# Performance work log

Hardware: AMD Instinct MI355X
Metric: run time of the kernel (lower is better)

Reference implementation:

```python
import jax, jax.numpy as jnp
import numpy as np

N, C, T, V = 32, 128, 256, 25
K = 5  # temporal kernel size; reflect-pad 2*(K-1)//2 = 4 rows on top
EPS = 1e-5


def _inorm(x):
    # InstanceNorm2d(affine=False): normalize each (n,c) plane over (T,V)
    m = jnp.mean(x, axis=(2, 3), keepdims=True)
    v = jnp.var(x, axis=(2, 3), keepdims=True)
    return (x - m) * jax.lax.rsqrt(v + EPS)


def setup_inputs() -> dict:
    key = jax.random.key(0)
    ks = jax.random.split(key, 5)
    x = jax.random.normal(ks[0], (N, C, T, V), jnp.float32)
    PA = jax.random.normal(ks[1], (V, V), jnp.float32)          # learned adjacency
    Wd = jax.random.normal(ks[2], (C, C), jnp.float32) * 0.05    # 1x1 conv weight (O,I)
    bd = jnp.zeros((C,), jnp.float32)
    Wt = jax.random.normal(ks[3], (C, C, K, 1), jnp.float32) * 0.02  # (O,I,Kt,1)
    bt = jnp.zeros((C,), jnp.float32)
    return {"x": x, "PA": PA, "Wd": Wd, "bd": bd, "Wt": Wt, "bt": bt}


def reference(x, PA, Wd, bd, Wt, bt):
    # GCN unit: x.view(N,C*T,V) @ PA == einsum over last (joint) axis
    g = jnp.einsum('nctv,vw->nctw', x, PA)
    # 1x1 conv (channel GEMM) + bias
    y = jnp.einsum('nctv,oc->notv', g, Wd) + bd[None, :, None, None]
    # instance norm + identity residual (in_c == out_c) + relu
    y = jax.nn.relu(_inorm(y) + x)
    # TCN unit: reflection-pad 4 rows on top of T, conv (5,1) stride 1, instance norm
    yp = jnp.pad(y, ((0, 0), (0, 0), (4, 0), (0, 0)), mode='reflect')
    z = jax.lax.conv_general_dilated(
        yp, Wt, window_strides=(1, 1), padding='VALID',
        dimension_numbers=('NCHW', 'OIHW', 'NCHW')) + bt[None, :, None, None]
    z = _inorm(z)
    # outer residual (identity: in_c == out_c, stride == 1) + relu
    return jax.nn.relu(z + x)
```

## Files before the change

### kernel.cpp

```cpp
#include <hip/hip_runtime.h>


typedef unsigned short u16;
typedef unsigned int   u32;

using short8  = __attribute__((ext_vector_type(8))) short;
using floatx4 = __attribute__((ext_vector_type(4))) float;

#define NBATCH 32
#define CH     128
#define TDIM   256
#define VDIM   25
#define KT     5
#define PLANE  6400
#define EPSF   1e-5f
#define INV_PLANE (1.0f/6400.0f)

__device__ __forceinline__ u16 f2bf(float f) {
    u32 u = __float_as_uint(f);
    return (u16)((u + 0x7fffu + ((u >> 16) & 1u)) >> 16);
}
__device__ __forceinline__ float bf2f(u16 h) {
    return __uint_as_float(((u32)h) << 16);
}
__device__ __forceinline__ void gload_lds16(const void* g, void* l) {
    __builtin_amdgcn_global_load_lds(
        (const __attribute__((address_space(1))) u32*)g,
        (__attribute__((address_space(3))) u32*)l, 16, 0, 0);
}

__global__ __launch_bounds__(256) void k0_init(
    const float* __restrict__ Wd, const float* __restrict__ Wt,
    float* __restrict__ statsY, float* __restrict__ statsZ,
    u16* __restrict__ WdB, u16* __restrict__ Wt_b)
{
    int i = blockIdx.x * 256 + threadIdx.x;
    if (i < 8192) {
        statsY[i] = 0.f;
    } else if (i < 16384) {
        statsZ[i - 8192] = 0.f;
    } else if (i < 32768) {
        int j  = i - 16384;
        int cl = j & 31;
        int o  = (j >> 5) & 127;
        int cc = j >> 12;
        WdB[j] = f2bf(Wd[o * CH + cc * 32 + cl]);
    } else {
        int j  = i - 32768;
        int il = j & 31;
        int o  = (j >> 5) & 127;
        int r2 = j >> 12;
        int tap = r2 % KT;
        int ic  = r2 / KT;
        Wt_b[j] = f2bf(Wt[(o * CH + ic * 32 + il) * KT + tap]);
    }
}

__global__ __launch_bounds__(256) void k1a_gcn(
    const float* __restrict__ x, const float* __restrict__ PA,
    u16* __restrict__ gT)
{
    __shared__ __attribute__((aligned(16))) u32 sG[6800];
    __shared__ float sPA[625];

    const int tid   = threadIdx.x;
    const int nic   = blockIdx.y;
    const int chunk = blockIdx.x;
    const int c0    = chunk * 400;
    const int cl    = tid >> 3;
    const int tl    = tid & 7;

    for (int i = tid; i < 625; i += 256) sPA[i] = PA[i];

    const float* xrow = x + (size_t)(nic * 32 + cl) * PLANE + c0 + tl * 50;
    float xr[50];
#pragma unroll
    for (int w = 0; w < 25; ++w) {
        float2 t2 = *(const float2*)(xrow + 2 * w);
        xr[2 * w]     = t2.x;
        xr[2 * w + 1] = t2.y;
    }
    __syncthreads();

    u16* sG16 = (u16*)sG;
#pragma unroll
    for (int v = 0; v < VDIM; ++v) {
        float g0 = 0.f, g1 = 0.f;
#pragma unroll
        for (int w = 0; w < VDIM; ++w) {
            float p = sPA[w * VDIM + v];
            g0 += xr[w] * p;
            g1 += xr[25 + w] * p;
        }
        int r0 = tl * 50 + v;
        sG16[r0 * 34 + cl]        = f2bf(g0);
        sG16[(r0 + 25) * 34 + cl] = f2bf(g1);
    }
    __syncthreads();

    u32* outd = (u32*)gT;
    const size_t ob = ((size_t)nic * PLANE + c0) * 16;
    for (int j = tid; j < 6400; j += 256) {
        int r = j >> 4, dw = j & 15;
        outd[ob + j] = sG[r * 17 + dw];
    }
}

__global__ __launch_bounds__(256) void k1b_mfma(
    const u16* __restrict__ gT, const u16* __restrict__ WdB,
    const float* __restrict__ bd,
    u16* __restrict__ y0b, float* __restrict__ statsY)
{
    __shared__ __attribute__((aligned(16))) char lds[65536];
    char* const sA = lds;
    char* const sB = lds + 32768;

    const int tid  = threadIdx.x;
    const int wave = tid >> 6;
    const int lane = tid & 63;
    const int l    = lane & 15;
    const int quad = lane >> 4;
    const int n    = blockIdx.y;
    const int c0   = blockIdx.x * 128;
    const int wub  = tid & ~63;

#pragma unroll
    for (int it = 0; it < 8; ++it)
        gload_lds16((const char*)WdB + (it * 256 + tid) * 16, sA + (it * 256 + wub) * 16);
#pragma unroll
    for (int cc = 0; cc < 4; ++cc) {
        const char* bsrc = (const char*)gT + ((size_t)(n * 4 + cc) * PLANE + c0) * 64;
#pragma unroll
        for (int it = 0; it < 2; ++it)
            gload_lds16(bsrc + (it * 256 + tid) * 16, sB + cc * 8192 + (it * 256 + wub) * 16);
    }
    __syncthreads();

    floatx4 acc[2][8];
#pragma unroll
    for (int a = 0; a < 2; ++a)
#pragma unroll
        for (int b = 0; b < 8; ++b) acc[a][b] = (floatx4){0.f, 0.f, 0.f, 0.f};

#pragma unroll
    for (int cc = 0; cc < 4; ++cc) {
        const short8 a0 = *(const short8*)(sA + cc * 8192 + (wave * 32      + l) * 64 + quad * 16);
        const short8 a1 = *(const short8*)(sA + cc * 8192 + (wave * 32 + 16 + l) * 64 + quad * 16);
#pragma unroll
        for (int ct = 0; ct < 8; ++ct) {
            const short8 b = *(const short8*)(sB + cc * 8192 + (ct * 16 + l) * 64 + quad * 16);
            acc[0][ct] = __builtin_amdgcn_mfma_f32_16x16x32_bf16(a0, b, acc[0][ct], 0, 0, 0);
            acc[1][ct] = __builtin_amdgcn_mfma_f32_16x16x32_bf16(a1, b, acc[1][ct], 0, 0, 0);
        }
    }

#pragma unroll
    for (int ot = 0; ot < 2; ++ot) {
#pragma unroll
        for (int reg = 0; reg < 4; ++reg) {
            const int o = wave * 32 + ot * 16 + quad * 4 + reg;
            const float bias = bd[o];
            float s1 = 0.f, s2 = 0.f;
            u16* yp = y0b + (size_t)(n * CH + o) * PLANE + c0 + l;
#pragma unroll
            for (int ct = 0; ct < 8; ++ct) {
                float val = acc[ot][ct][reg] + bias;
                yp[ct * 16] = f2bf(val);
                s1 += val; s2 += val * val;
            }
#pragma unroll
            for (int m = 1; m <= 8; m <<= 1) {
                s1 += __shfl_xor(s1, m, 64);
                s2 += __shfl_xor(s2, m, 64);
            }
            if (l == 0) {
                atomicAdd(&statsY[(n * CH + o) * 2 + 0], s1);
                atomicAdd(&statsY[(n * CH + o) * 2 + 1], s2);
            }
        }
    }
}

__global__ __launch_bounds__(256) void k2_yhat(
    const u16* __restrict__ y0b, const float* __restrict__ x,
    const float* __restrict__ statsY, u16* __restrict__ yhatT)
{
    __shared__ u32 sT[256 * 17];
    __shared__ float sM[32], sR[32];

    const int tid = threadIdx.x;
    const int nic = blockIdx.y;
    const int n   = nic >> 2, ic = nic & 3;
    const int c0  = blockIdx.x * 256;

    if (tid < 32) {
        float a = statsY[(n * CH + ic * 32 + tid) * 2 + 0];
        float b = statsY[(n * CH + ic * 32 + tid) * 2 + 1];
        float m = a * INV_PLANE;
        sM[tid] = m;
        sR[tid] = rsqrtf(b * INV_PLANE - m * m + EPSF);
    }
    __syncthreads();

    for (int idx = tid; idx < 4096; idx += 256) {
        int ip = idx >> 8;
        int c  = idx & 255;
        int i0 = ip * 2;
        int g0 = (n * CH + ic * 32 + i0) * PLANE + c0 + c;
        int g1 = g0 + PLANE;
        float va = fmaxf((bf2f(y0b[g0]) - sM[i0]) * sR[i0] + x[g0], 0.f);
        float vb = fmaxf((bf2f(y0b[g1]) - sM[i0 + 1]) * sR[i0 + 1] + x[g1], 0.f);
        sT[c * 17 + ip] = (u32)f2bf(va) | ((u32)f2bf(vb) << 16);
    }
    __syncthreads();

    u32* outd = (u32*)yhatT;
    int obase = (nic * PLANE + c0) * 16;
    for (int idx = tid; idx < 4096; idx += 256)
        outd[obase + idx] = sT[(idx >> 4) * 17 + (idx & 15)];
}

__global__ __launch_bounds__(256) void k3_mfma(
    const u16* __restrict__ yhatT, const u16* __restrict__ Wt_b,
    const float* __restrict__ bt,
    float* __restrict__ zout, float* __restrict__ statsZ)
{
    __shared__ __attribute__((aligned(16))) char lds[57344];
    char* const sB = lds;
    char* const sA = lds + 16384;

    const int tid  = threadIdx.x;
    const int wave = tid >> 6;
    const int lane = tid & 63;
    const int l    = lane & 15;
    const int quad = lane >> 4;
    const int n    = blockIdx.y;
    const int blk  = blockIdx.x;
    const int c0   = blk * 128;
    const int wub  = tid & ~63;

    floatx4 acc[2][8];
#pragma unroll
    for (int a = 0; a < 2; ++a)
#pragma unroll
        for (int b = 0; b < 8; ++b) acc[a][b] = (floatx4){0.f, 0.f, 0.f, 0.f};

    for (int ic = 0; ic < 4; ++ic) {
        __syncthreads();
        const char* asrc = (const char*)(Wt_b + ic * 20480);
#pragma unroll
        for (int it = 0; it < 10; ++it)
            gload_lds16(asrc + (it * 256 + tid) * 16, sA + (it * 256 + wub) * 16);
        const char* bsrc = (const char*)(yhatT + (size_t)(n * 4 + ic) * (PLANE * 32));
        if (blk == 0) {
#pragma unroll
            for (int it = 0; it < 2; ++it)
                gload_lds16(bsrc + (it * 256 + tid) * 16, sB + 6400 + (it * 256 + wub) * 16);
            const u32* bsrcd = (const u32*)bsrc;
            u32* sBd = (u32*)sB;
            for (int idx = tid; idx < 1600; idx += 256) {
                int r = idx >> 4, dw = idx & 15;
                int d = 100 - r;
                int tref = (d + 24) / 25;
                int v = r % 25;
                sBd[idx] = bsrcd[(tref * 25 + v) * 16 + dw];
            }
        } else {
            const char* bsrc2 = bsrc + (size_t)(c0 - 100) * 64;
#pragma unroll
            for (int it = 0; it < 4; ++it)
                gload_lds16(bsrc2 + (it * 256 + tid) * 16, sB + (it * 256 + wub) * 16);
        }
        __syncthreads();
#pragma unroll
        for (int tap = 0; tap < KT; ++tap) {
            const short8 a0 = *(const short8*)(sA + tap * 8192 + (wave * 32      + l) * 64 + quad * 16);
            const short8 a1 = *(const short8*)(sA + tap * 8192 + (wave * 32 + 16 + l) * 64 + quad * 16);
#pragma unroll
            for (int ct = 0; ct < 8; ++ct) {
                const short8 b = *(const short8*)(sB + (ct * 16 + l + tap * 25) * 64 + quad * 16);
                acc[0][ct] = __builtin_amdgcn_mfma_f32_16x16x32_bf16(a0, b, acc[0][ct], 0, 0, 0);
                acc[1][ct] = __builtin_amdgcn_mfma_f32_16x16x32_bf16(a1, b, acc[1][ct], 0, 0, 0);
            }
        }
    }

#pragma unroll
    for (int ot = 0; ot < 2; ++ot) {
#pragma unroll
        for (int reg = 0; reg < 4; ++reg) {
            const int o = wave * 32 + ot * 16 + quad * 4 + reg;
            const float bias = bt[o];
            float s1 = 0.f, s2 = 0.f;
            float* zp = zout + (size_t)(n * CH + o) * PLANE + c0 + l;
#pragma unroll
            for (int ct = 0; ct < 8; ++ct) {
                float val = acc[ot][ct][reg] + bias;
                zp[ct * 16] = val;
                s1 += val; s2 += val * val;
            }
#pragma unroll
            for (int m = 1; m <= 8; m <<= 1) {
                s1 += __shfl_xor(s1, m, 64);
                s2 += __shfl_xor(s2, m, 64);
            }
            if (l == 0) {
                atomicAdd(&statsZ[(n * CH + o) * 2 + 0], s1);
                atomicAdd(&statsZ[(n * CH + o) * 2 + 1], s2);
            }
        }
    }
}

__global__ __launch_bounds__(256) void k4_final(
    const float* __restrict__ x, const float* __restrict__ statsZ,
    float* __restrict__ out)
{
    int i4 = blockIdx.x * 256 + threadIdx.x;
    int p  = i4 / 1600;
    float a = statsZ[p * 2 + 0], b = statsZ[p * 2 + 1];
    float m = a * INV_PLANE;
    float r = rsqrtf(b * INV_PLANE - m * m + EPSF);
    float4 z  = ((const float4*)out)[i4];
    float4 xv = ((const float4*)x)[i4];
    float4 o;
    o.x = fmaxf((z.x - m) * r + xv.x, 0.f);
    o.y = fmaxf((z.y - m) * r + xv.y, 0.f);
    o.z = fmaxf((z.z - m) * r + xv.z, 0.f);
    o.w = fmaxf((z.w - m) * r + xv.w, 0.f);
    ((float4*)out)[i4] = o;
}

extern "C" void kernel_launch(void* const* d_in, const int* in_sizes, int n_in,
                              void* d_out, int out_size, void* d_ws, size_t ws_size,
                              hipStream_t stream) {
    const float* x  = (const float*)d_in[0];
    const float* PA = (const float*)d_in[1];
    const float* Wd = (const float*)d_in[2];
    const float* bd = (const float*)d_in[3];
    const float* Wt = (const float*)d_in[4];
    const float* bt = (const float*)d_in[5];
    float* out = (float*)d_out;

    char* wsb = (char*)d_ws;
    u16*   y0b    = (u16*)(wsb);
    u16*   gT     = (u16*)(wsb + 52428800);
    u16*   yhatT  = gT;
    float* statsY = (float*)(wsb + 104857600);
    float* statsZ = (float*)(wsb + 104890368);
    u16*   WdB    = (u16*)(wsb + 104923136);
    u16*   Wt_b   = (u16*)(wsb + 104955904);

    k0_init<<<dim3(448), dim3(256), 0, stream>>>(Wd, Wt, statsY, statsZ, WdB, Wt_b);
    k1a_gcn<<<dim3(16, 128), dim3(256), 0, stream>>>(x, PA, gT);
    k1b_mfma<<<dim3(50, 32), dim3(256), 0, stream>>>(gT, WdB, bd, y0b, statsY);
    k2_yhat<<<dim3(25, 128), dim3(256), 0, stream>>>(y0b, x, statsY, yhatT);
    k3_mfma<<<dim3(50, 32), dim3(256), 0, stream>>>(yhatT, Wt_b, bt, out, statsZ);
    k4_final<<<dim3(25600), dim3(256), 0, stream>>>(x, statsZ, out);
}
```

Baseline: 382.9 us.

## Swizzle LDS layouts, enlarge k3 tile, store conv output as bf16

```diff
diff --git a/kernel.cpp b/kernel.cpp
--- a/kernel.cpp
+++ b/kernel.cpp
@@ -41,17 +41,19 @@
         statsZ[i - 8192] = 0.f;
     } else if (i < 32768) {
         int j  = i - 16384;
-        int cl = j & 31;
+        int sl = j & 31;
         int o  = (j >> 5) & 127;
         int cc = j >> 12;
+        int cl = (((sl >> 3) ^ (o & 3)) << 3) | (sl & 7);
         WdB[j] = f2bf(Wd[o * CH + cc * 32 + cl]);
     } else {
         int j  = i - 32768;
-        int il = j & 31;
+        int sl = j & 31;
         int o  = (j >> 5) & 127;
         int r2 = j >> 12;
         int tap = r2 % KT;
         int ic  = r2 / KT;
+        int il = (((sl >> 3) ^ (o & 3)) << 3) | (sl & 7);
         Wt_b[j] = f2bf(Wt[(o * CH + ic * 32 + il) * KT + tap]);
     }
 }
@@ -102,7 +104,8 @@
     const size_t ob = ((size_t)nic * PLANE + c0) * 16;
     for (int j = tid; j < 6400; j += 256) {
         int r = j >> 4, dw = j & 15;
-        outd[ob + j] = sG[r * 17 + dw];
+        int q = dw >> 2, b = dw & 3;
+        outd[ob + r * 16 + (((q ^ (r & 3)) << 2) | b)] = sG[r * 17 + dw];
     }
 }
 
@@ -142,13 +145,14 @@
 #pragma unroll
         for (int b = 0; b < 8; ++b) acc[a][b] = (floatx4){0.f, 0.f, 0.f, 0.f};
 
+    const int swzA = (quad ^ (l & 3)) << 4;
 #pragma unroll
     for (int cc = 0; cc < 4; ++cc) {
-        const short8 a0 = *(const short8*)(sA + cc * 8192 + (wave * 32      + l) * 64 + quad * 16);
-        const short8 a1 = *(const short8*)(sA + cc * 8192 + (wave * 32 + 16 + l) * 64 + quad * 16);
+        const short8 a0 = *(const short8*)(sA + cc * 8192 + (wave * 32      + l) * 64 + swzA);
+        const short8 a1 = *(const short8*)(sA + cc * 8192 + (wave * 32 + 16 + l) * 64 + swzA);
 #pragma unroll
         for (int ct = 0; ct < 8; ++ct) {
-            const short8 b = *(const short8*)(sB + cc * 8192 + (ct * 16 + l) * 64 + quad * 16);
+            const short8 b = *(const short8*)(sB + cc * 8192 + (ct * 16 + l) * 64 + swzA);
             acc[0][ct] = __builtin_amdgcn_mfma_f32_16x16x32_bf16(a0, b, acc[0][ct], 0, 0, 0);
             acc[1][ct] = __builtin_amdgcn_mfma_f32_16x16x32_bf16(a1, b, acc[1][ct], 0, 0, 0);
         }
@@ -216,32 +220,37 @@
 
     u32* outd = (u32*)yhatT;
     int obase = (nic * PLANE + c0) * 16;
-    for (int idx = tid; idx < 4096; idx += 256)
-        outd[obase + idx] = sT[(idx >> 4) * 17 + (idx & 15)];
-}
-
-__global__ __launch_bounds__(256) void k3_mfma(
+    for (int idx = tid; idx < 4096; idx += 256) {
+        int r = idx >> 4, dw = idx & 15;
+        int q = dw >> 2, b = dw & 3;
+        outd[obase + r * 16 + (((q ^ (r & 3)) << 2) | b)] = sT[r * 17 + dw];
+    }
+}
+
+__global__ __launch_bounds__(256, 2) void k3_mfma(
     const u16* __restrict__ yhatT, const u16* __restrict__ Wt_b,
     const float* __restrict__ bt,
-    float* __restrict__ zout, float* __restrict__ statsZ)
-{
-    __shared__ __attribute__((aligned(16))) char lds[57344];
+    u16* __restrict__ zb, float* __restrict__ statsZ)
+{
+    __shared__ __attribute__((aligned(16))) char lds[65536];
     char* const sB = lds;
-    char* const sA = lds + 16384;
+    char* const sA = lds + 24576;
 
     const int tid  = threadIdx.x;
     const int wave = tid >> 6;
+    const int wr   = wave >> 1;
+    const int wc   = wave & 1;
     const int lane = tid & 63;
     const int l    = lane & 15;
     const int quad = lane >> 4;
     const int n    = blockIdx.y;
     const int blk  = blockIdx.x;
-    const int c0   = blk * 128;
+    const int c0   = blk * 256;
     const int wub  = tid & ~63;
 
-    floatx4 acc[2][8];
-#pragma unroll
-    for (int a = 0; a < 2; ++a)
+    floatx4 acc[4][8];
+#pragma unroll
+    for (int a = 0; a < 4; ++a)
 #pragma unroll
         for (int b = 0; b < 8; ++b) acc[a][b] = (floatx4){0.f, 0.f, 0.f, 0.f};
 
@@ -254,49 +263,58 @@
         const char* bsrc = (const char*)(yhatT + (size_t)(n * 4 + ic) * (PLANE * 32));
         if (blk == 0) {
 #pragma unroll
-            for (int it = 0; it < 2; ++it)
+            for (int it = 0; it < 4; ++it)
                 gload_lds16(bsrc + (it * 256 + tid) * 16, sB + 6400 + (it * 256 + wub) * 16);
             const u32* bsrcd = (const u32*)bsrc;
             u32* sBd = (u32*)sB;
             for (int idx = tid; idx < 1600; idx += 256) {
                 int r = idx >> 4, dw = idx & 15;
+                int q = dw >> 2, b = dw & 3;
                 int d = 100 - r;
                 int tref = (d + 24) / 25;
                 int v = r % 25;
-                sBd[idx] = bsrcd[(tref * 25 + v) * 16 + dw];
+                int sc = tref * 25 + v;
+                sBd[r * 16 + (((q ^ (r & 3)) << 2) | b)] =
+                    bsrcd[sc * 16 + (((q ^ (sc & 3)) << 2) | b)];
             }
         } else {
             const char* bsrc2 = bsrc + (size_t)(c0 - 100) * 64;
 #pragma unroll
-            for (int it = 0; it < 4; ++it)
+            for (int it = 0; it < 6; ++it)
                 gload_lds16(bsrc2 + (it * 256 + tid) * 16, sB + (it * 256 + wub) * 16);
         }
         __syncthreads();
 #pragma unroll
         for (int tap = 0; tap < KT; ++tap) {
-            const short8 a0 = *(const short8*)(sA + tap * 8192 + (wave * 32      + l) * 64 + quad * 16);
-            const short8 a1 = *(const short8*)(sA + tap * 8192 + (wave * 32 + 16 + l) * 64 + quad * 16);
+            short8 af[4];
+#pragma unroll
+            for (int ot = 0; ot < 4; ++ot) {
+                int ro = wr * 64 + ot * 16 + l;
+                af[ot] = *(const short8*)(sA + tap * 8192 + ro * 64 + ((quad ^ (l & 3)) << 4));
+            }
 #pragma unroll
             for (int ct = 0; ct < 8; ++ct) {
-                const short8 b = *(const short8*)(sB + (ct * 16 + l + tap * 25) * 64 + quad * 16);
-                acc[0][ct] = __builtin_amdgcn_mfma_f32_16x16x32_bf16(a0, b, acc[0][ct], 0, 0, 0);
-                acc[1][ct] = __builtin_amdgcn_mfma_f32_16x16x32_bf16(a1, b, acc[1][ct], 0, 0, 0);
-            }
-        }
-    }
-
-#pragma unroll
-    for (int ot = 0; ot < 2; ++ot) {
+                int r = wc * 128 + ct * 16 + l + tap * 25;
+                const short8 b = *(const short8*)(sB + r * 64 + ((quad ^ (r & 3)) << 4));
+#pragma unroll
+                for (int ot = 0; ot < 4; ++ot)
+                    acc[ot][ct] = __builtin_amdgcn_mfma_f32_16x16x32_bf16(af[ot], b, acc[ot][ct], 0, 0, 0);
+            }
+        }
+    }
+
+#pragma unroll
+    for (int ot = 0; ot < 4; ++ot) {
 #pragma unroll
         for (int reg = 0; reg < 4; ++reg) {
-            const int o = wave * 32 + ot * 16 + quad * 4 + reg;
+            const int o = wr * 64 + ot * 16 + quad * 4 + reg;
             const float bias = bt[o];
             float s1 = 0.f, s2 = 0.f;
-            float* zp = zout + (size_t)(n * CH + o) * PLANE + c0 + l;
+            u16* zp = zb + (size_t)(n * CH + o) * PLANE + c0 + wc * 128 + l;
 #pragma unroll
             for (int ct = 0; ct < 8; ++ct) {
                 float val = acc[ot][ct][reg] + bias;
-                zp[ct * 16] = val;
+                zp[ct * 16] = f2bf(val);
                 s1 += val; s2 += val * val;
             }
 #pragma unroll
@@ -313,22 +331,29 @@
 }
 
 __global__ __launch_bounds__(256) void k4_final(
-    const float* __restrict__ x, const float* __restrict__ statsZ,
-    float* __restrict__ out)
-{
-    int i4 = blockIdx.x * 256 + threadIdx.x;
-    int p  = i4 / 1600;
+    const u16* __restrict__ zb, const float* __restrict__ x,
+    const float* __restrict__ statsZ, float* __restrict__ out)
+{
+    int g = blockIdx.x * 256 + threadIdx.x;
+    int p = g / 800;
     float a = statsZ[p * 2 + 0], b = statsZ[p * 2 + 1];
     float m = a * INV_PLANE;
     float r = rsqrtf(b * INV_PLANE - m * m + EPSF);
-    float4 z  = ((const float4*)out)[i4];
-    float4 xv = ((const float4*)x)[i4];
-    float4 o;
-    o.x = fmaxf((z.x - m) * r + xv.x, 0.f);
-    o.y = fmaxf((z.y - m) * r + xv.y, 0.f);
-    o.z = fmaxf((z.z - m) * r + xv.z, 0.f);
-    o.w = fmaxf((z.w - m) * r + xv.w, 0.f);
-    ((float4*)out)[i4] = o;
+    short8 zv = *(const short8*)(zb + (size_t)g * 8);
+    const float4* xp = (const float4*)x + (size_t)g * 2;
+    float4 x0 = xp[0], x1 = xp[1];
+    float4 o0, o1;
+    o0.x = fmaxf((bf2f((u16)zv[0]) - m) * r + x0.x, 0.f);
+    o0.y = fmaxf((bf2f((u16)zv[1]) - m) * r + x0.y, 0.f);
+    o0.z = fmaxf((bf2f((u16)zv[2]) - m) * r + x0.z, 0.f);
+    o0.w = fmaxf((bf2f((u16)zv[3]) - m) * r + x0.w, 0.f);
+    o1.x = fmaxf((bf2f((u16)zv[4]) - m) * r + x1.x, 0.f);
+    o1.y = fmaxf((bf2f((u16)zv[5]) - m) * r + x1.y, 0.f);
+    o1.z = fmaxf((bf2f((u16)zv[6]) - m) * r + x1.z, 0.f);
+    o1.w = fmaxf((bf2f((u16)zv[7]) - m) * r + x1.w, 0.f);
+    float4* op = (float4*)out + (size_t)g * 2;
+    op[0] = o0;
+    op[1] = o1;
 }
 
 extern "C" void kernel_launch(void* const* d_in, const int* in_sizes, int n_in,
@@ -344,6 +369,7 @@
 
     char* wsb = (char*)d_ws;
     u16*   y0b    = (u16*)(wsb);
+    u16*   zb     = y0b;
     u16*   gT     = (u16*)(wsb + 52428800);
     u16*   yhatT  = gT;
     float* statsY = (float*)(wsb + 104857600);
@@ -355,6 +381,6 @@
     k1a_gcn<<<dim3(16, 128), dim3(256), 0, stream>>>(x, PA, gT);
     k1b_mfma<<<dim3(50, 32), dim3(256), 0, stream>>>(gT, WdB, bd, y0b, statsY);
     k2_yhat<<<dim3(25, 128), dim3(256), 0, stream>>>(y0b, x, statsY, yhatT);
-    k3_mfma<<<dim3(50, 32), dim3(256), 0, stream>>>(yhatT, Wt_b, bt, out, statsZ);
-    k4_final<<<dim3(25600), dim3(256), 0, stream>>>(x, statsZ, out);
-}
+    k3_mfma<<<dim3(25, 32), dim3(256), 0, stream>>>(yhatT, Wt_b, bt, zb, statsZ);
+    k4_final<<<dim3(12800), dim3(256), 0, stream>>>(zb, x, statsZ, out);
+}
```

After: 375.1 us. -2.0%, faster.
